# Kernel tuning notes

Hardware: AMD Instinct MI355X
Metric: run time of the kernel (lower is better)

## Reference

```python
import jax, jax.numpy as jnp
import numpy as np

EPS = 1e-5

def layernorm(x, g, b):
    mu = jnp.mean(x, axis=-1, keepdims=True)
    var = jnp.mean(jnp.square(x - mu), axis=-1, keepdims=True)
    return (x - mu) * jax.lax.rsqrt(var + EPS) * g + b

def setup_inputs() -> dict:
    key = jax.random.key(0)
    ks = jax.random.split(key, 12)
    B, T, C, H = 4, 2048, 1024, 8
    Dh = C // H          # 128
    Dff = 4 * C          # 4096
    s = 0.02
    return {
        "x":     jax.random.normal(ks[0], (B, T, C), jnp.float32),
        "wq":    jax.random.normal(ks[1], (H, C, Dh), jnp.float32) * s,
        "wk":    jax.random.normal(ks[2], (H, C, Dh), jnp.float32) * s,
        "wv":    jax.random.normal(ks[3], (H, C, Dh), jnp.float32) * s,
        "w1":    jax.random.normal(ks[4], (C, Dff), jnp.float32) * s,
        "b1":    jnp.zeros((Dff,), jnp.float32),
        "w2":    jax.random.normal(ks[5], (Dff, C), jnp.float32) * s,
        "b2":    jnp.zeros((C,), jnp.float32),
        "ln1_g": jnp.ones((C,), jnp.float32),
        "ln1_b": jnp.zeros((C,), jnp.float32),
        "ln2_g": jnp.ones((C,), jnp.float32),
        "ln2_b": jnp.zeros((C,), jnp.float32),
    }

def reference(x, wq, wk, wv, w1, b1, w2, b2, ln1_g, ln1_b, ln2_g, ln2_b):
    B, T, C = x.shape
    H, _, Dh = wq.shape
    # --- multi-head self-attention (pre-LN) ---
    h = layernorm(x, ln1_g, ln1_b)
    q = jnp.einsum("btc,hcd->bhtd", h, wq)
    k = jnp.einsum("btc,hcd->bhtd", h, wk)
    v = jnp.einsum("btc,hcd->bhtd", h, wv)
    # NOTE: original multiplies by sqrt(head_size) (not divide) -- kept faithful
    scores = jnp.einsum("bhtd,bhsd->bhts", q, k) * (Dh ** 0.5)
    attn = jax.nn.softmax(scores, axis=-1)
    # dropout(p=0.2) treated as identity (eval mode)
    o = jnp.einsum("bhts,bhsd->bhtd", attn, v)
    # concat heads along last dim: head h fills contiguous slice
    o = o.transpose(0, 2, 1, 3).reshape(B, T, H * Dh)
    x = x + o  # no output projection in original module
    # --- feed-forward (pre-LN) ---
    h2 = layernorm(x, ln2_g, ln2_b)
    ff = jax.nn.relu(h2 @ w1 + b1) @ w2 + b2
    return x + ff
```

## Files before the change

kernel.cpp:

```cpp
#include <hip/hip_runtime.h>
#include <hip/hip_bf16.h>
#include <math.h>

#define B_   4
#define T_   2048
#define C_   1024
#define H_   8
#define DH   128
#define DFF  4096
#define M_   (B_*T_)

typedef __attribute__((ext_vector_type(8))) short bf16x8;
typedef __attribute__((ext_vector_type(4))) float f32x4;
typedef __attribute__((ext_vector_type(2))) unsigned int u32x2;

#define SC2 16.32223094f

__device__ __forceinline__ unsigned short f2bf(float x) {
  union { float f; unsigned u; } v; v.f = x;
  return (unsigned short)((v.u + 0x7fffu + ((v.u >> 16) & 1u)) >> 16);
}
__device__ __forceinline__ float bf2f(unsigned short h) {
  union { unsigned u; float f; } v; v.u = ((unsigned)h) << 16; return v.f;
}

__device__ __forceinline__ f32x4 mfma_bf16(bf16x8 a, bf16x8 b, f32x4 c) {
  return __builtin_amdgcn_mfma_f32_16x16x32_bf16(a, b, c, 0, 0, 0);
}

__device__ __forceinline__ void gll16(const void* g, void* l) {
  __builtin_amdgcn_global_load_lds((const __attribute__((address_space(1))) void*)g,
                                   (__attribute__((address_space(3))) void*)l,
                                   16, 0, 0);
}

__global__ __launch_bounds__(256) void ln_kernel(const float* __restrict__ in,
                                                 const float* __restrict__ g,
                                                 const float* __restrict__ bb,
                                                 unsigned short* __restrict__ h_hi,
                                                 unsigned short* __restrict__ h_lo) {
  __shared__ float red[8];
  const int row = blockIdx.x;
  const int tid = threadIdx.x;
  const float* p = in + (size_t)row * C_;
  const float4 xv = *(const float4*)(p + (tid << 2));
  float s  = xv.x + xv.y + xv.z + xv.w;
  float sq = xv.x*xv.x + xv.y*xv.y + xv.z*xv.z + xv.w*xv.w;
  #pragma unroll
  for (int off = 32; off > 0; off >>= 1) {
    s  += __shfl_xor(s, off);
    sq += __shfl_xor(sq, off);
  }
  if ((tid & 63) == 0) { red[(tid >> 6) * 2] = s; red[(tid >> 6) * 2 + 1] = sq; }
  __syncthreads();
  s  = red[0] + red[2] + red[4] + red[6];
  sq = red[1] + red[3] + red[5] + red[7];
  const float mu  = s * (1.0f / C_);
  const float var = sq * (1.0f / C_) - mu * mu;
  const float rs  = rsqrtf(var + 1e-5f);
  const float4 gv = *(const float4*)(g  + (tid << 2));
  const float4 bv = *(const float4*)(bb + (tid << 2));
  float ov[4];
  ov[0] = (xv.x - mu) * rs * gv.x + bv.x;
  ov[1] = (xv.y - mu) * rs * gv.y + bv.y;
  ov[2] = (xv.z - mu) * rs * gv.z + bv.z;
  ov[3] = (xv.w - mu) * rs * gv.w + bv.w;
  ushort4 hv, lv;
  unsigned short* hp = (unsigned short*)&hv;
  unsigned short* lp = (unsigned short*)&lv;
  #pragma unroll
  for (int j = 0; j < 4; ++j) {
    hp[j] = f2bf(ov[j]);
    lp[j] = f2bf(ov[j] - bf2f(hp[j]));
  }
  *(ushort4*)(h_hi + (size_t)row * C_ + (tid << 2)) = hv;
  *(ushort4*)(h_lo + (size_t)row * C_ + (tid << 2)) = lv;
}

__global__ __launch_bounds__(256) void cvt_t_kernel(const float* __restrict__ in,
                                                    unsigned short* __restrict__ out,
                                                    int R, int CC) {
  __shared__ float tile[32][33];
  const int r0 = blockIdx.y << 5, c0 = blockIdx.x << 5;
  const int tr = threadIdx.x >> 3, tc4 = (threadIdx.x & 7) << 2;
  const float4 vv = *(const float4*)(in + (size_t)(r0 + tr) * CC + c0 + tc4);
  tile[tr][tc4+0] = vv.x; tile[tr][tc4+1] = vv.y;
  tile[tr][tc4+2] = vv.z; tile[tr][tc4+3] = vv.w;
  __syncthreads();
  ushort4 o;
  o.x = f2bf(tile[tc4+0][tr]); o.y = f2bf(tile[tc4+1][tr]);
  o.z = f2bf(tile[tc4+2][tr]); o.w = f2bf(tile[tc4+3][tr]);
  *(ushort4*)(out + (size_t)(c0 + tr) * R + r0 + tc4) = o;
}

__global__ __launch_bounds__(256) void cvt_qkv_kernel(const float* __restrict__ wq,
                                                      const float* __restrict__ wk,
                                                      const float* __restrict__ wv,
                                                      unsigned short* __restrict__ wt_hi,
                                                      unsigned short* __restrict__ wt_lo) {
  const int z = blockIdx.z;
  const int which = z >> 3, head = z & 7;
  const float* in = (which == 0 ? wq : (which == 1 ? wk : wv)) + (size_t)head * C_ * DH;
  unsigned short* oh = wt_hi + (size_t)z * DH * C_;
  unsigned short* ol = wt_lo + (size_t)z * DH * C_;
  __shared__ float tile[32][33];
  const int r0 = blockIdx.y << 5, c0 = blockIdx.x << 5;
  const int tr = threadIdx.x >> 3, tc4 = (threadIdx.x & 7) << 2;
  const float4 vv = *(const float4*)(in + (size_t)(r0 + tr) * DH + c0 + tc4);
  tile[tr][tc4+0] = vv.x; tile[tr][tc4+1] = vv.y;
  tile[tr][tc4+2] = vv.z; tile[tr][tc4+3] = vv.w;
  __syncthreads();
  ushort4 hv, lv;
  unsigned short* hp = (unsigned short*)&hv;
  unsigned short* lp = (unsigned short*)&lv;
  #pragma unroll
  for (int j = 0; j < 4; ++j) {
    const float val = tile[tc4+j][tr];
    hp[j] = f2bf(val);
    lp[j] = f2bf(val - bf2f(hp[j]));
  }
  *(ushort4*)(oh + (size_t)(c0 + tr) * C_ + r0 + tc4) = hv;
  *(ushort4*)(ol + (size_t)(c0 + tr) * C_ + r0 + tc4) = lv;
}

template<int TERMS>
__device__ __forceinline__ void gemm128_mfma(
    const unsigned short* __restrict__ Ah, const unsigned short* __restrict__ Al,
    int lda,
    const unsigned short* __restrict__ Bh, const unsigned short* __restrict__ Bl,
    int ldb, int K, f32x4 (&acc)[4][4],
    unsigned short* AhS, unsigned short* AlS,
    unsigned short* BhS, unsigned short* BlS) {
  const int tid  = threadIdx.x;
  const int w    = tid >> 6;
  const int lane = tid & 63;
  const int l15  = lane & 15, quad = lane >> 4;
  const int srow = lane >> 2, skc = (lane & 3) << 3;
  const int wm = w & 1, wn = w >> 1;

  for (int k0 = 0; k0 < K; k0 += 32) {
    __syncthreads();
    #pragma unroll
    for (int i = 0; i < 2; ++i) {
      const int seg  = w * 2 + i;
      const int r    = seg * 16 + srow;
      const int lofs = seg * 512 + lane * 8;
      gll16(Ah + (size_t)r * lda + k0 + skc, AhS + lofs);
      gll16(Bh + (size_t)r * ldb + k0 + skc, BhS + lofs);
      if (TERMS == 3) {
        gll16(Al + (size_t)r * lda + k0 + skc, AlS + lofs);
        gll16(Bl + (size_t)r * ldb + k0 + skc, BlS + lofs);
      }
    }
    __syncthreads();
    bf16x8 aH[4], bH[4], aL[4], bL[4];
    #pragma unroll
    for (int t = 0; t < 4; ++t) {
      aH[t] = *(const bf16x8*)&AhS[(wm * 64 + t * 16 + l15) * 32 + quad * 8];
      bH[t] = *(const bf16x8*)&BhS[(wn * 64 + t * 16 + l15) * 32 + quad * 8];
      if (TERMS == 3) {
        aL[t] = *(const bf16x8*)&AlS[(wm * 64 + t * 16 + l15) * 32 + quad * 8];
        bL[t] = *(const bf16x8*)&BlS[(wn * 64 + t * 16 + l15) * 32 + quad * 8];
      }
    }
    #pragma unroll
    for (int rt = 0; rt < 4; ++rt)
      #pragma unroll
      for (int ct = 0; ct < 4; ++ct) {
        if (TERMS == 3) {
          acc[rt][ct] = mfma_bf16(aL[rt], bH[ct], acc[rt][ct]);
          acc[rt][ct] = mfma_bf16(aH[rt], bL[ct], acc[rt][ct]);
        }
        acc[rt][ct] = mfma_bf16(aH[rt], bH[ct], acc[rt][ct]);
      }
  }
}

__global__ __launch_bounds__(256) void qkm_kernel(const unsigned short* __restrict__ h_hi,
                                                  const unsigned short* __restrict__ h_lo,
                                                  const unsigned short* __restrict__ wt_hi,
                                                  const unsigned short* __restrict__ wt_lo,
                                                  unsigned short* __restrict__ q_hi,
                                                  unsigned short* __restrict__ q_lo,
                                                  unsigned short* __restrict__ k_hi,
                                                  unsigned short* __restrict__ k_lo) {
  __shared__ __align__(16) unsigned short AhS[4096], AlS[4096];
  __shared__ __align__(16) unsigned short BhS[4096], BlS[4096];
  const int m0 = blockIdx.x << 7;
  const int z  = blockIdx.y;
  const int which = z >> 3, head = z & 7;
  f32x4 acc[4][4];
  #pragma unroll
  for (int i = 0; i < 4; ++i)
    #pragma unroll
    for (int j = 0; j < 4; ++j)
      #pragma unroll
      for (int r = 0; r < 4; ++r) acc[i][j][r] = 0.f;
  gemm128_mfma<3>(h_hi + (size_t)m0 * C_, h_lo + (size_t)m0 * C_, C_,
                  wt_hi + (size_t)z * DH * C_, wt_lo + (size_t)z * DH * C_, C_,
                  C_, acc, AhS, AlS, BhS, BlS);
  const int lane = threadIdx.x & 63, w = threadIdx.x >> 6;
  const int l15 = lane & 15, quad = lane >> 4;
  const int wm = w & 1, wn = w >> 1;
  const int bh = (m0 >> 11) * H_ + head;
  const int tbase = (m0 & (T_ - 1)) + wm * 64 + quad * 4;
  if (which == 0) {
    #pragma unroll
    for (int rt = 0; rt < 4; ++rt)
      #pragma unroll
      for (int ct = 0; ct < 4; ++ct) {
        const int d = wn * 64 + ct * 16 + l15;
        #pragma unroll
        for (int r = 0; r < 4; ++r) {
          const int t = tbase + rt * 16 + r;
          const float val = acc[rt][ct][r] * SC2;
          const unsigned short hb = f2bf(val);
          const size_t idx = ((size_t)bh * T_ + t) * DH + d;
          q_hi[idx] = hb;
          q_lo[idx] = f2bf(val - bf2f(hb));
        }
      }
  } else {
    #pragma unroll
    for (int rt = 0; rt < 4; ++rt)
      #pragma unroll
      for (int ct = 0; ct < 4; ++ct) {
        const int d = wn * 64 + ct * 16 + l15;
        #pragma unroll
        for (int r = 0; r < 4; ++r) {
          const int t = tbase + rt * 16 + r;
          const float val = acc[rt][ct][r];
          const unsigned short hb = f2bf(val);
          const size_t idx = (((size_t)bh * 64 + (t >> 5)) * 4 + (d >> 5)) * 1024
                           + (size_t)(t & 31) * 32 + (d & 31);
          k_hi[idx] = hb;
          k_lo[idx] = f2bf(val - bf2f(hb));
        }
      }
  }
}

__global__ __launch_bounds__(256) void vm_kernel(const unsigned short* __restrict__ h_hi,
                                                 const unsigned short* __restrict__ wv_hi,
                                                 unsigned short* __restrict__ vimg) {
  __shared__ __align__(16) unsigned short AhS[4096], BhS[4096];
  const int m0 = blockIdx.x << 7;
  const int head = blockIdx.y;
  f32x4 acc[4][4];
  #pragma unroll
  for (int i = 0; i < 4; ++i)
    #pragma unroll
    for (int j = 0; j < 4; ++j)
      #pragma unroll
      for (int r = 0; r < 4; ++r) acc[i][j][r] = 0.f;
  gemm128_mfma<1>(h_hi + (size_t)m0 * C_, nullptr, C_,
                  wv_hi + (size_t)(16 + head) * DH * C_, nullptr, C_,
                  C_, acc, AhS, nullptr, BhS, nullptr);
  const int lane = threadIdx.x & 63, w = threadIdx.x >> 6;
  const int l15 = lane & 15, quad = lane >> 4;
  const int wm = w & 1, wn = w >> 1;
  const int bh = (m0 >> 11) * H_ + head;
  #pragma unroll
  for (int rt = 0; rt < 4; ++rt)
    #pragma unroll
    for (int ct = 0; ct < 4; ++ct) {
      const int d  = wn * 64 + ct * 16 + l15;
      const int t0 = (m0 & (T_ - 1)) + wm * 64 + rt * 16 + quad * 4;
      ushort4 pk;
      pk.x = f2bf(acc[rt][ct][0]); pk.y = f2bf(acc[rt][ct][1]);
      pk.z = f2bf(acc[rt][ct][2]); pk.w = f2bf(acc[rt][ct][3]);
      *(ushort4*)&vimg[(((size_t)bh * 64 + (t0 >> 5)) * 128 + d) * 32 + (t0 & 31)] = pk;
    }
}

__global__ __launch_bounds__(256) void ff1_kernel(const unsigned short* __restrict__ h2,
                                                  const unsigned short* __restrict__ w1t,
                                                  const float* __restrict__ b1,
                                                  unsigned short* __restrict__ ff1) {
  __shared__ __align__(16) unsigned short AhS[4096], BhS[4096];
  const int n0 = blockIdx.x << 7;
  const int m0 = blockIdx.y << 7;
  f32x4 acc[4][4];
  #pragma unroll
  for (int i = 0; i < 4; ++i)
    #pragma unroll
    for (int j = 0; j < 4; ++j)
      #pragma unroll
      for (int r = 0; r < 4; ++r) acc[i][j][r] = 0.f;
  gemm128_mfma<1>(h2 + (size_t)m0 * C_, nullptr, C_,
                  w1t + (size_t)n0 * C_, nullptr, C_,
                  C_, acc, AhS, nullptr, BhS, nullptr);
  const int lane = threadIdx.x & 63, w = threadIdx.x >> 6;
  const int l15 = lane & 15, quad = lane >> 4;
  const int wm = w & 1, wn = w >> 1;
  #pragma unroll
  for (int rt = 0; rt < 4; ++rt)
    #pragma unroll
    for (int ct = 0; ct < 4; ++ct) {
      const int n = n0 + wn * 64 + ct * 16 + l15;
      const float bias = b1[n];
      #pragma unroll
      for (int r = 0; r < 4; ++r) {
        const int m = m0 + wm * 64 + rt * 16 + quad * 4 + r;
        ff1[(size_t)m * DFF + n] = f2bf(fmaxf(acc[rt][ct][r] + bias, 0.f));
      }
    }
}

__global__ __launch_bounds__(256) void ff2_kernel(const unsigned short* __restrict__ ff1,
                                                  const unsigned short* __restrict__ w2t,
                                                  const float* __restrict__ b2,
                                                  const float* __restrict__ xo,
                                                  float* __restrict__ out) {
  __shared__ __align__(16) unsigned short AhS[4096], BhS[4096];
  const int n0 = blockIdx.x << 7;
  const int m0 = blockIdx.y << 7;
  f32x4 acc[4][4];
  #pragma unroll
  for (int i = 0; i < 4; ++i)
    #pragma unroll
    for (int j = 0; j < 4; ++j)
      #pragma unroll
      for (int r = 0; r < 4; ++r) acc[i][j][r] = 0.f;
  gemm128_mfma<1>(ff1 + (size_t)m0 * DFF, nullptr, DFF,
                  w2t + (size_t)n0 * DFF, nullptr, DFF,
                  DFF, acc, AhS, nullptr, BhS, nullptr);
  const int lane = threadIdx.x & 63, w = threadIdx.x >> 6;
  const int l15 = lane & 15, quad = lane >> 4;
  const int wm = w & 1, wn = w >> 1;
  #pragma unroll
  for (int rt = 0; rt < 4; ++rt)
    #pragma unroll
    for (int ct = 0; ct < 4; ++ct) {
      const int n = n0 + wn * 64 + ct * 16 + l15;
      const float bias = b2[n];
      #pragma unroll
      for (int r = 0; r < 4; ++r) {
        const int m = m0 + wm * 64 + rt * 16 + quad * 4 + r;
        out[(size_t)m * C_ + n] = acc[rt][ct][r] + bias + xo[(size_t)m * C_ + n];
      }
    }
}

#define BQ 128

__global__ __launch_bounds__(256, 2) void attn_kernel(
    const unsigned short* __restrict__ q_hi, const unsigned short* __restrict__ q_lo,
    const unsigned short* __restrict__ k_hi, const unsigned short* __restrict__ k_lo,
    const unsigned short* __restrict__ vimg,
    const float* __restrict__ x, float* __restrict__ xo) {
  __shared__ __align__(16) unsigned short KhS[8192];
  __shared__ __align__(16) unsigned short KlS[8192];
  __shared__ __align__(16) unsigned short VtS[8192];
  __shared__ __align__(16) unsigned short PS [8192];

  const int bh  = blockIdx.y;
  const int qt0 = blockIdx.x * BQ;
  const int tid  = threadIdx.x;
  const int w    = tid >> 6;
  const int lane = tid & 63;
  const int l15  = lane & 15;
  const int quad = lane >> 4;
  const int srcbase = quad * 20;

  bf16x8 Qh[2][4], Ql[2][4];
  #pragma unroll
  for (int rt = 0; rt < 2; ++rt) {
    const int row = qt0 + w * 32 + rt * 16 + l15;
    #pragma unroll
    for (int kc = 0; kc < 4; ++kc) {
      const size_t off = ((size_t)bh * T_ + row) * DH + kc * 32 + quad * 8;
      Qh[rt][kc] = *(const bf16x8*)(q_hi + off);
      Ql[rt][kc] = *(const bf16x8*)(q_lo + off);
    }
  }

  f32x4 O[2][8];
  #pragma unroll
  for (int rt = 0; rt < 2; ++rt)
    #pragma unroll
    for (int n = 0; n < 8; ++n)
      #pragma unroll
      for (int r = 0; r < 4; ++r) O[rt][n][r] = 0.f;
  float m_cur[2] = { -1e30f, -1e30f };
  float l_cur[2] = { 0.f, 0.f };

  for (int kt = 0; kt < T_ / 64; ++kt) {
    const size_t tb = ((size_t)bh * 64 + kt * 2) * 4096;
    __syncthreads();
    #pragma unroll
    for (int i = 0; i < 4; ++i) {
      const int ofs = (w * 4 + i) * 512 + lane * 8;
      gll16(k_hi + tb + ofs, KhS + ofs);
      gll16(k_lo + tb + ofs, KlS + ofs);
      gll16(vimg + tb + ofs, VtS + ofs);
    }
    __syncthreads();

    f32x4 S[4][2];
    #pragma unroll
    for (int ct = 0; ct < 4; ++ct)
      #pragma unroll
      for (int rt = 0; rt < 2; ++rt)
        #pragma unroll
        for (int r = 0; r < 4; ++r) S[ct][rt][r] = 0.f;
    __builtin_amdgcn_s_setprio(1);
    #pragma unroll
    for (int kc = 0; kc < 4; ++kc) {
      #pragma unroll
      for (int ct = 0; ct < 4; ++ct) {
        const int o = (ct >> 1) * 4096 + kc * 1024 + (((ct & 1) << 4) + l15) * 32 + quad * 8;
        const bf16x8 kh = *(const bf16x8*)&KhS[o];
        const bf16x8 kl = *(const bf16x8*)&KlS[o];
        #pragma unroll
        for (int rt = 0; rt < 2; ++rt) {
          S[ct][rt] = mfma_bf16(kl, Qh[rt][kc], S[ct][rt]);
          S[ct][rt] = mfma_bf16(kh, Ql[rt][kc], S[ct][rt]);
          S[ct][rt] = mfma_bf16(kh, Qh[rt][kc], S[ct][rt]);
        }
      }
    }
    __builtin_amdgcn_s_setprio(0);

    float mx[2];
    #pragma unroll
    for (int rt = 0; rt < 2; ++rt) {
      const float c0 = fmaxf(fmaxf(S[0][rt][0], S[0][rt][1]), fmaxf(S[0][rt][2], S[0][rt][3]));
      const float c1 = fmaxf(fmaxf(S[1][rt][0], S[1][rt][1]), fmaxf(S[1][rt][2], S[1][rt][3]));
      const float c2 = fmaxf(fmaxf(S[2][rt][0], S[2][rt][1]), fmaxf(S[2][rt][2], S[2][rt][3]));
      const float c3 = fmaxf(fmaxf(S[3][rt][0], S[3][rt][1]), fmaxf(S[3][rt][2], S[3][rt][3]));
      float m0 = fmaxf(fmaxf(c0, c1), fmaxf(c2, c3));
      m0 = fmaxf(m0, __shfl_xor(m0, 16));
      m0 = fmaxf(m0, __shfl_xor(m0, 32));
      mx[rt] = m0;
    }

    const int need = (mx[0] > m_cur[0] + 8.f) || (mx[1] > m_cur[1] + 8.f);
    if (__any(need)) {
      #pragma unroll
      for (int rt = 0; rt < 2; ++rt) {
        const float mn = fmaxf(m_cur[rt], mx[rt]);
        const float al = exp2f(m_cur[rt] - mn);
        m_cur[rt] = mn;
        l_cur[rt] *= al;
        #pragma unroll
        for (int r = 0; r < 4; ++r) {
          const float ar = __shfl(al, srcbase + r);
          #pragma unroll
          for (int n = 0; n < 8; ++n) O[rt][n][r] *= ar;
        }
      }
    }

    #pragma unroll
    for (int rt = 0; rt < 2; ++rt) {
      const int rowb = (w * 32 + rt * 16 + l15) * 128;
      float rs = 0.f;
      #pragma unroll
      for (int ct = 0; ct < 4; ++ct) {
        const float p0 = exp2f(S[ct][rt][0] - m_cur[rt]);
        const float p1 = exp2f(S[ct][rt][1] - m_cur[rt]);
        const float p2 = exp2f(S[ct][rt][2] - m_cur[rt]);
        const float p3 = exp2f(S[ct][rt][3] - m_cur[rt]);
        rs += (p0 + p1) + (p2 + p3);
        u32x2 uu;
        uu.x = (__float_as_uint(p1) & 0xffff0000u) | (__float_as_uint(p0) >> 16);
        uu.y = (__float_as_uint(p3) & 0xffff0000u) | (__float_as_uint(p2) >> 16);
        const int slot = (ct * 2 + (quad >> 1)) ^ (l15 & 7);
        *(u32x2*)((char*)PS + rowb + (slot << 4) + ((quad & 1) << 3)) = uu;
      }
      rs += __shfl_xor(rs, 16);
      rs += __shfl_xor(rs, 32);
      l_cur[rt] += rs;
    }

    __builtin_amdgcn_s_setprio(1);
    #pragma unroll
    for (int kc = 0; kc < 2; ++kc) {
      bf16x8 aP[2];
      #pragma unroll
      for (int rt = 0; rt < 2; ++rt) {
        const int rowb = (w * 32 + rt * 16 + l15) * 128;
        const int slot = (kc * 4 + quad) ^ (l15 & 7);
        aP[rt] = *(const bf16x8*)((const char*)PS + rowb + (slot << 4));
      }
      #pragma unroll
      for (int n = 0; n < 8; ++n) {
        const bf16x8 bv = *(const bf16x8*)&VtS[kc * 4096 + (n * 16 + l15) * 32 + quad * 8];
        O[0][n] = mfma_bf16(aP[0], bv, O[0][n]);
        O[1][n] = mfma_bf16(aP[1], bv, O[1][n]);
      }
    }
    __builtin_amdgcn_s_setprio(0);
  }

  const int b = bh >> 3, hh = bh & 7;
  #pragma unroll
  for (int rt = 0; rt < 2; ++rt) {
    #pragma unroll
    for (int r = 0; r < 4; ++r) {
      const float lr = __shfl(l_cur[rt], srcbase + r);
      const float inv_l = 1.0f / lr;
      const int t = qt0 + w * 32 + rt * 16 + quad * 4 + r;
      const size_t xrow = ((size_t)(b * T_ + t)) * C_ + (size_t)hh * DH;
      #pragma unroll
      for (int n = 0; n < 8; ++n) {
        const int d = n * 16 + l15;
        xo[xrow + d] = x[xrow + d] + O[rt][n][r] * inv_l;
      }
    }
  }
}

extern "C" void kernel_launch(void* const* d_in, const int* in_sizes, int n_in,
                              void* d_out, int out_size, void* d_ws, size_t ws_size,
                              hipStream_t stream) {
  (void)in_sizes; (void)n_in; (void)out_size; (void)ws_size;
  const float* x     = (const float*)d_in[0];
  const float* wq    = (const float*)d_in[1];
  const float* wk    = (const float*)d_in[2];
  const float* wv    = (const float*)d_in[3];
  const float* w1    = (const float*)d_in[4];
  const float* b1    = (const float*)d_in[5];
  const float* w2    = (const float*)d_in[6];
  const float* b2    = (const float*)d_in[7];
  const float* ln1_g = (const float*)d_in[8];
  const float* ln1_b = (const float*)d_in[9];
  const float* ln2_g = (const float*)d_in[10];
  const float* ln2_b = (const float*)d_in[11];
  float* out = (float*)d_out;

  char* W = (char*)d_ws;
  float* xo = (float*)(W);
  unsigned short* q_hi  = (unsigned short*)(W + (32u  << 20));
  unsigned short* q_lo  = (unsigned short*)(W + (48u  << 20));
  unsigned short* k_hi  = (unsigned short*)(W + (64u  << 20));
  unsigned short* k_lo  = (unsigned short*)(W + (80u  << 20));
  unsigned short* vimg  = (unsigned short*)(W + (96u  << 20));
  unsigned short* ff1   = (unsigned short*)(W + (32u  << 20));
  unsigned short* h_hi  = (unsigned short*)(W + (112u << 20));
  unsigned short* h_lo  = (unsigned short*)(W + (128u << 20));
  unsigned short* w1t   = (unsigned short*)(W + (144u << 20));
  unsigned short* w2t   = (unsigned short*)(W + (152u << 20));
  unsigned short* wt_hi = (unsigned short*)(W + (160u << 20));
  unsigned short* wt_lo = (unsigned short*)(W + (166u << 20));

  cvt_t_kernel<<<dim3(DFF / 32, C_ / 32), 256, 0, stream>>>(w1, w1t, C_, DFF);
  cvt_t_kernel<<<dim3(C_ / 32, DFF / 32), 256, 0, stream>>>(w2, w2t, DFF, C_);
  cvt_qkv_kernel<<<dim3(DH / 32, C_ / 32, 24), 256, 0, stream>>>(wq, wk, wv, wt_hi, wt_lo);
  ln_kernel<<<M_, 256, 0, stream>>>(x, ln1_g, ln1_b, h_hi, h_lo);
  qkm_kernel<<<dim3(M_ / 128, 16), 256, 0, stream>>>(h_hi, h_lo, wt_hi, wt_lo,
                                                     q_hi, q_lo, k_hi, k_lo);
  vm_kernel<<<dim3(M_ / 128, H_), 256, 0, stream>>>(h_hi, wt_hi, vimg);
  attn_kernel<<<dim3(T_ / BQ, B_ * H_), 256, 0, stream>>>(q_hi, q_lo, k_hi, k_lo,
                                                          vimg, x, xo);
  ln_kernel<<<M_, 256, 0, stream>>>(xo, ln2_g, ln2_b, h_hi, h_lo);
  ff1_kernel<<<dim3(DFF / 128, M_ / 128), 256, 0, stream>>>(h_hi, w1t, b1, ff1);
  ff2_kernel<<<dim3(C_ / 128, M_ / 128), 256, 0, stream>>>(ff1, w2t, b2, xo, out);
}
```

Baseline: 616.5 us.

## Double-buffer GEMM and attention LDS tiles with XOR swizzle and block remap

Adds a double-buffered bf16 GEMM path (used for the V projection and both FFN GEMMs) that prefetches the next K-slice into a second LDS buffer while computing the current one. The flash-attention loop is reworked the same way, with 32-key tiles ping-ponged across two buffers. XOR swizzles are applied to LDS layouts and to the K/V global images to reduce bank conflicts, and attention blocks are remapped so consecutive blocks spread across heads. The extra LDS per block may lower occupancy, and the wrap-around prefetch on the last iteration loads data that is never used.

```diff
diff --git a/kernel.cpp b/kernel.cpp
--- a/kernel.cpp
+++ b/kernel.cpp
@@ -123,8 +123,8 @@
   *(ushort4*)(ol + (size_t)(c0 + tr) * C_ + r0 + tc4) = lv;
 }
 
-template<int TERMS>
-__device__ __forceinline__ void gemm128_mfma(
+
+__device__ __forceinline__ void gemm128_split3(
     const unsigned short* __restrict__ Ah, const unsigned short* __restrict__ Al,
     int lda,
     const unsigned short* __restrict__ Bh, const unsigned short* __restrict__ Bl,
@@ -135,8 +135,10 @@
   const int w    = tid >> 6;
   const int lane = tid & 63;
   const int l15  = lane & 15, quad = lane >> 4;
-  const int srow = lane >> 2, skc = (lane & 3) << 3;
+  const int srow = lane >> 2;
+  const int skc  = ((lane & 3) << 3) ^ (((srow >> 1) & 3) << 3);
   const int wm = w & 1, wn = w >> 1;
+  const int ro = ((quad ^ ((l15 >> 1) & 3)) << 3);
 
   for (int k0 = 0; k0 < K; k0 += 32) {
     __syncthreads();
@@ -147,32 +149,76 @@
       const int lofs = seg * 512 + lane * 8;
       gll16(Ah + (size_t)r * lda + k0 + skc, AhS + lofs);
       gll16(Bh + (size_t)r * ldb + k0 + skc, BhS + lofs);
-      if (TERMS == 3) {
-        gll16(Al + (size_t)r * lda + k0 + skc, AlS + lofs);
-        gll16(Bl + (size_t)r * ldb + k0 + skc, BlS + lofs);
-      }
+      gll16(Al + (size_t)r * lda + k0 + skc, AlS + lofs);
+      gll16(Bl + (size_t)r * ldb + k0 + skc, BlS + lofs);
     }
     __syncthreads();
     bf16x8 aH[4], bH[4], aL[4], bL[4];
     #pragma unroll
     for (int t = 0; t < 4; ++t) {
-      aH[t] = *(const bf16x8*)&AhS[(wm * 64 + t * 16 + l15) * 32 + quad * 8];
-      bH[t] = *(const bf16x8*)&BhS[(wn * 64 + t * 16 + l15) * 32 + quad * 8];
-      if (TERMS == 3) {
-        aL[t] = *(const bf16x8*)&AlS[(wm * 64 + t * 16 + l15) * 32 + quad * 8];
-        bL[t] = *(const bf16x8*)&BlS[(wn * 64 + t * 16 + l15) * 32 + quad * 8];
-      }
+      aH[t] = *(const bf16x8*)&AhS[(wm * 64 + t * 16 + l15) * 32 + ro];
+      bH[t] = *(const bf16x8*)&BhS[(wn * 64 + t * 16 + l15) * 32 + ro];
+      aL[t] = *(const bf16x8*)&AlS[(wm * 64 + t * 16 + l15) * 32 + ro];
+      bL[t] = *(const bf16x8*)&BlS[(wn * 64 + t * 16 + l15) * 32 + ro];
     }
     #pragma unroll
     for (int rt = 0; rt < 4; ++rt)
       #pragma unroll
       for (int ct = 0; ct < 4; ++ct) {
-        if (TERMS == 3) {
-          acc[rt][ct] = mfma_bf16(aL[rt], bH[ct], acc[rt][ct]);
-          acc[rt][ct] = mfma_bf16(aH[rt], bL[ct], acc[rt][ct]);
-        }
+        acc[rt][ct] = mfma_bf16(aL[rt], bH[ct], acc[rt][ct]);
+        acc[rt][ct] = mfma_bf16(aH[rt], bL[ct], acc[rt][ct]);
         acc[rt][ct] = mfma_bf16(aH[rt], bH[ct], acc[rt][ct]);
       }
+  }
+}
+
+__device__ __forceinline__ void gemm128_db(
+    const unsigned short* __restrict__ Ah, int lda,
+    const unsigned short* __restrict__ Bh, int ldb, int K, f32x4 (&acc)[4][4],
+    unsigned short (&AS0)[4096], unsigned short (&AS1)[4096],
+    unsigned short (&BS0)[4096], unsigned short (&BS1)[4096]) {
+  const int tid  = threadIdx.x;
+  const int w    = tid >> 6;
+  const int lane = tid & 63;
+  const int l15  = lane & 15, quad = lane >> 4;
+  const int srow = lane >> 2;
+  const int skc  = ((lane & 3) << 3) ^ (((srow >> 1) & 3) << 3);
+  const int wm = w & 1, wn = w >> 1;
+  const int ro = ((quad ^ ((l15 >> 1) & 3)) << 3);
+  const int Km = K - 1;
+
+  auto STG = [&](int k0, unsigned short* A, unsigned short* B) {
+    #pragma unroll
+    for (int i = 0; i < 2; ++i) {
+      const int seg  = w * 2 + i;
+      const int r    = seg * 16 + srow;
+      const int lofs = seg * 512 + lane * 8;
+      gll16(Ah + (size_t)r * lda + k0 + skc, A + lofs);
+      gll16(Bh + (size_t)r * ldb + k0 + skc, B + lofs);
+    }
+  };
+  auto CMP = [&](const unsigned short* A, const unsigned short* B) {
+    bf16x8 aH[4], bH[4];
+    #pragma unroll
+    for (int t = 0; t < 4; ++t) {
+      aH[t] = *(const bf16x8*)&A[(wm * 64 + t * 16 + l15) * 32 + ro];
+      bH[t] = *(const bf16x8*)&B[(wn * 64 + t * 16 + l15) * 32 + ro];
+    }
+    #pragma unroll
+    for (int rt = 0; rt < 4; ++rt)
+      #pragma unroll
+      for (int ct = 0; ct < 4; ++ct)
+        acc[rt][ct] = mfma_bf16(aH[rt], bH[ct], acc[rt][ct]);
+  };
+
+  STG(0, AS0, BS0);
+  for (int k0 = 0; k0 < K; k0 += 64) {
+    __syncthreads();
+    STG((k0 + 32) & Km, AS1, BS1);
+    CMP(AS0, BS0);
+    __syncthreads();
+    STG((k0 + 64) & Km, AS0, BS0);
+    CMP(AS1, BS1);
   }
 }
 
@@ -196,9 +242,9 @@
     for (int j = 0; j < 4; ++j)
       #pragma unroll
       for (int r = 0; r < 4; ++r) acc[i][j][r] = 0.f;
-  gemm128_mfma<3>(h_hi + (size_t)m0 * C_, h_lo + (size_t)m0 * C_, C_,
-                  wt_hi + (size_t)z * DH * C_, wt_lo + (size_t)z * DH * C_, C_,
-                  C_, acc, AhS, AlS, BhS, BlS);
+  gemm128_split3(h_hi + (size_t)m0 * C_, h_lo + (size_t)m0 * C_, C_,
+                 wt_hi + (size_t)z * DH * C_, wt_lo + (size_t)z * DH * C_, C_,
+                 C_, acc, AhS, AlS, BhS, BlS);
   const int lane = threadIdx.x & 63, w = threadIdx.x >> 6;
   const int l15 = lane & 15, quad = lane >> 4;
   const int wm = w & 1, wn = w >> 1;
@@ -229,10 +275,11 @@
         #pragma unroll
         for (int r = 0; r < 4; ++r) {
           const int t = tbase + rt * 16 + r;
+          const int tt = t & 31;
           const float val = acc[rt][ct][r];
           const unsigned short hb = f2bf(val);
           const size_t idx = (((size_t)bh * 64 + (t >> 5)) * 4 + (d >> 5)) * 1024
-                           + (size_t)(t & 31) * 32 + (d & 31);
+                           + (size_t)tt * 32 + ((d & 31) ^ (((tt >> 1) & 3) << 3));
           k_hi[idx] = hb;
           k_lo[idx] = f2bf(val - bf2f(hb));
         }
@@ -243,7 +290,8 @@
 __global__ __launch_bounds__(256) void vm_kernel(const unsigned short* __restrict__ h_hi,
                                                  const unsigned short* __restrict__ wv_hi,
                                                  unsigned short* __restrict__ vimg) {
-  __shared__ __align__(16) unsigned short AhS[4096], BhS[4096];
+  __shared__ __align__(16) unsigned short AS0[4096], AS1[4096];
+  __shared__ __align__(16) unsigned short BS0[4096], BS1[4096];
   const int m0 = blockIdx.x << 7;
   const int head = blockIdx.y;
   f32x4 acc[4][4];
@@ -253,9 +301,9 @@
     for (int j = 0; j < 4; ++j)
       #pragma unroll
       for (int r = 0; r < 4; ++r) acc[i][j][r] = 0.f;
-  gemm128_mfma<1>(h_hi + (size_t)m0 * C_, nullptr, C_,
-                  wv_hi + (size_t)(16 + head) * DH * C_, nullptr, C_,
-                  C_, acc, AhS, nullptr, BhS, nullptr);
+  gemm128_db(h_hi + (size_t)m0 * C_, C_,
+             wv_hi + (size_t)(16 + head) * DH * C_, C_,
+             C_, acc, AS0, AS1, BS0, BS1);
   const int lane = threadIdx.x & 63, w = threadIdx.x >> 6;
   const int l15 = lane & 15, quad = lane >> 4;
   const int wm = w & 1, wn = w >> 1;
@@ -266,10 +314,11 @@
     for (int ct = 0; ct < 4; ++ct) {
       const int d  = wn * 64 + ct * 16 + l15;
       const int t0 = (m0 & (T_ - 1)) + wm * 64 + rt * 16 + quad * 4;
+      const int key = (t0 & 31) ^ (((d >> 1) & 3) << 3);
       ushort4 pk;
       pk.x = f2bf(acc[rt][ct][0]); pk.y = f2bf(acc[rt][ct][1]);
       pk.z = f2bf(acc[rt][ct][2]); pk.w = f2bf(acc[rt][ct][3]);
-      *(ushort4*)&vimg[(((size_t)bh * 64 + (t0 >> 5)) * 128 + d) * 32 + (t0 & 31)] = pk;
+      *(ushort4*)&vimg[(((size_t)bh * 64 + (t0 >> 5)) * 128 + d) * 32 + key] = pk;
     }
 }
 
@@ -277,7 +326,8 @@
                                                   const unsigned short* __restrict__ w1t,
                                                   const float* __restrict__ b1,
                                                   unsigned short* __restrict__ ff1) {
-  __shared__ __align__(16) unsigned short AhS[4096], BhS[4096];
+  __shared__ __align__(16) unsigned short AS0[4096], AS1[4096];
+  __shared__ __align__(16) unsigned short BS0[4096], BS1[4096];
   const int n0 = blockIdx.x << 7;
   const int m0 = blockIdx.y << 7;
   f32x4 acc[4][4];
@@ -287,9 +337,9 @@
     for (int j = 0; j < 4; ++j)
       #pragma unroll
       for (int r = 0; r < 4; ++r) acc[i][j][r] = 0.f;
-  gemm128_mfma<1>(h2 + (size_t)m0 * C_, nullptr, C_,
-                  w1t + (size_t)n0 * C_, nullptr, C_,
-                  C_, acc, AhS, nullptr, BhS, nullptr);
+  gemm128_db(h2 + (size_t)m0 * C_, C_,
+             w1t + (size_t)n0 * C_, C_,
+             C_, acc, AS0, AS1, BS0, BS1);
   const int lane = threadIdx.x & 63, w = threadIdx.x >> 6;
   const int l15 = lane & 15, quad = lane >> 4;
   const int wm = w & 1, wn = w >> 1;
@@ -312,7 +362,8 @@
                                                   const float* __restrict__ b2,
                                                   const float* __restrict__ xo,
                                                   float* __restrict__ out) {
-  __shared__ __align__(16) unsigned short AhS[4096], BhS[4096];
+  __shared__ __align__(16) unsigned short AS0[4096], AS1[4096];
+  __shared__ __align__(16) unsigned short BS0[4096], BS1[4096];
   const int n0 = blockIdx.x << 7;
   const int m0 = blockIdx.y << 7;
   f32x4 acc[4][4];
@@ -322,9 +373,9 @@
     for (int j = 0; j < 4; ++j)
       #pragma unroll
       for (int r = 0; r < 4; ++r) acc[i][j][r] = 0.f;
-  gemm128_mfma<1>(ff1 + (size_t)m0 * DFF, nullptr, DFF,
-                  w2t + (size_t)n0 * DFF, nullptr, DFF,
-                  DFF, acc, AhS, nullptr, BhS, nullptr);
+  gemm128_db(ff1 + (size_t)m0 * DFF, DFF,
+             w2t + (size_t)n0 * DFF, DFF,
+             DFF, acc, AS0, AS1, BS0, BS1);
   const int lane = threadIdx.x & 63, w = threadIdx.x >> 6;
   const int l15 = lane & 15, quad = lane >> 4;
   const int wm = w & 1, wn = w >> 1;
@@ -349,18 +400,22 @@
     const unsigned short* __restrict__ k_hi, const unsigned short* __restrict__ k_lo,
     const unsigned short* __restrict__ vimg,
     const float* __restrict__ x, float* __restrict__ xo) {
-  __shared__ __align__(16) unsigned short KhS[8192];
-  __shared__ __align__(16) unsigned short KlS[8192];
-  __shared__ __align__(16) unsigned short VtS[8192];
-  __shared__ __align__(16) unsigned short PS [8192];
-
-  const int bh  = blockIdx.y;
-  const int qt0 = blockIdx.x * BQ;
+  __shared__ __align__(16) unsigned short Kh0[4096], Kh1[4096];
+  __shared__ __align__(16) unsigned short Kl0[4096], Kl1[4096];
+  __shared__ __align__(16) unsigned short Vt0[4096], Vt1[4096];
+  __shared__ __align__(16) unsigned short PS [4096];
+
+  const int bid   = blockIdx.x + (T_ / BQ) * blockIdx.y;
+  const int chunk = bid >> 3;
+  const int bh    = (bid & 7) * 4 + (chunk >> 4);
+  const int qt0   = (chunk & 15) * BQ;
+
   const int tid  = threadIdx.x;
   const int w    = tid >> 6;
   const int lane = tid & 63;
   const int l15  = lane & 15;
   const int quad = lane >> 4;
+  const int swz  = (l15 >> 1) & 3;
   const int srcbase = quad * 20;
 
   bf16x8 Qh[2][4], Ql[2][4];
@@ -385,21 +440,23 @@
   float m_cur[2] = { -1e30f, -1e30f };
   float l_cur[2] = { 0.f, 0.f };
 
-  for (int kt = 0; kt < T_ / 64; ++kt) {
-    const size_t tb = ((size_t)bh * 64 + kt * 2) * 4096;
-    __syncthreads();
-    #pragma unroll
-    for (int i = 0; i < 4; ++i) {
-      const int ofs = (w * 4 + i) * 512 + lane * 8;
-      gll16(k_hi + tb + ofs, KhS + ofs);
-      gll16(k_lo + tb + ofs, KlS + ofs);
-      gll16(vimg + tb + ofs, VtS + ofs);
-    }
-    __syncthreads();
-
-    f32x4 S[4][2];
-    #pragma unroll
-    for (int ct = 0; ct < 4; ++ct)
+  auto STAGE = [&](int kt, unsigned short* KH, unsigned short* KL,
+                   unsigned short* VT) {
+    const size_t tb = ((size_t)bh * 64 + kt) * 4096;
+    #pragma unroll
+    for (int i = 0; i < 2; ++i) {
+      const int ofs = (w * 2 + i) * 512 + lane * 8;
+      gll16(k_hi + tb + ofs, KH + ofs);
+      gll16(k_lo + tb + ofs, KL + ofs);
+      gll16(vimg + tb + ofs, VT + ofs);
+    }
+  };
+
+  auto TILE = [&](const unsigned short* KH, const unsigned short* KL,
+                  const unsigned short* VT) {
+    f32x4 S[2][2];
+    #pragma unroll
+    for (int ct = 0; ct < 2; ++ct)
       #pragma unroll
       for (int rt = 0; rt < 2; ++rt)
         #pragma unroll
@@ -408,10 +465,10 @@
     #pragma unroll
     for (int kc = 0; kc < 4; ++kc) {
       #pragma unroll
-      for (int ct = 0; ct < 4; ++ct) {
-        const int o = (ct >> 1) * 4096 + kc * 1024 + (((ct & 1) << 4) + l15) * 32 + quad * 8;
-        const bf16x8 kh = *(const bf16x8*)&KhS[o];
-        const bf16x8 kl = *(const bf16x8*)&KlS[o];
+      for (int ct = 0; ct < 2; ++ct) {
+        const int o = kc * 1024 + (ct * 16 + l15) * 32 + ((quad ^ swz) << 3);
+        const bf16x8 kh = *(const bf16x8*)&KH[o];
+        const bf16x8 kl = *(const bf16x8*)&KL[o];
         #pragma unroll
         for (int rt = 0; rt < 2; ++rt) {
           S[ct][rt] = mfma_bf16(kl, Qh[rt][kc], S[ct][rt]);
@@ -425,11 +482,11 @@
     float mx[2];
     #pragma unroll
     for (int rt = 0; rt < 2; ++rt) {
-      const float c0 = fmaxf(fmaxf(S[0][rt][0], S[0][rt][1]), fmaxf(S[0][rt][2], S[0][rt][3]));
-      const float c1 = fmaxf(fmaxf(S[1][rt][0], S[1][rt][1]), fmaxf(S[1][rt][2], S[1][rt][3]));
-      const float c2 = fmaxf(fmaxf(S[2][rt][0], S[2][rt][1]), fmaxf(S[2][rt][2], S[2][rt][3]));
-      const float c3 = fmaxf(fmaxf(S[3][rt][0], S[3][rt][1]), fmaxf(S[3][rt][2], S[3][rt][3]));
-      float m0 = fmaxf(fmaxf(c0, c1), fmaxf(c2, c3));
+      const float a = fmaxf(fmaxf(S[0][rt][0], S[0][rt][1]),
+                            fmaxf(S[0][rt][2], S[0][rt][3]));
+      const float b = fmaxf(fmaxf(S[1][rt][0], S[1][rt][1]),
+                            fmaxf(S[1][rt][2], S[1][rt][3]));
+      float m0 = fmaxf(a, b);
       m0 = fmaxf(m0, __shfl_xor(m0, 16));
       m0 = fmaxf(m0, __shfl_xor(m0, 32));
       mx[rt] = m0;
@@ -454,10 +511,10 @@
 
     #pragma unroll
     for (int rt = 0; rt < 2; ++rt) {
-      const int rowb = (w * 32 + rt * 16 + l15) * 128;
+      const int rowb = (w * 32 + rt * 16 + l15) * 64;
       float rs = 0.f;
       #pragma unroll
-      for (int ct = 0; ct < 4; ++ct) {
+      for (int ct = 0; ct < 2; ++ct) {
         const float p0 = exp2f(S[ct][rt][0] - m_cur[rt]);
         const float p1 = exp2f(S[ct][rt][1] - m_cur[rt]);
         const float p2 = exp2f(S[ct][rt][2] - m_cur[rt]);
@@ -466,7 +523,7 @@
         u32x2 uu;
         uu.x = (__float_as_uint(p1) & 0xffff0000u) | (__float_as_uint(p0) >> 16);
         uu.y = (__float_as_uint(p3) & 0xffff0000u) | (__float_as_uint(p2) >> 16);
-        const int slot = (ct * 2 + (quad >> 1)) ^ (l15 & 7);
+        const int slot = (ct * 2 + (quad >> 1)) ^ swz;
         *(u32x2*)((char*)PS + rowb + (slot << 4) + ((quad & 1) << 3)) = uu;
       }
       rs += __shfl_xor(rs, 16);
@@ -474,24 +531,32 @@
       l_cur[rt] += rs;
     }
 
+    bf16x8 aP[2];
+    #pragma unroll
+    for (int rt = 0; rt < 2; ++rt) {
+      const int rowb = (w * 32 + rt * 16 + l15) * 64;
+      aP[rt] = *(const bf16x8*)((const char*)PS + rowb + ((quad ^ swz) << 4));
+    }
     __builtin_amdgcn_s_setprio(1);
     #pragma unroll
-    for (int kc = 0; kc < 2; ++kc) {
-      bf16x8 aP[2];
-      #pragma unroll
-      for (int rt = 0; rt < 2; ++rt) {
-        const int rowb = (w * 32 + rt * 16 + l15) * 128;
-        const int slot = (kc * 4 + quad) ^ (l15 & 7);
-        aP[rt] = *(const bf16x8*)((const char*)PS + rowb + (slot << 4));
-      }
-      #pragma unroll
-      for (int n = 0; n < 8; ++n) {
-        const bf16x8 bv = *(const bf16x8*)&VtS[kc * 4096 + (n * 16 + l15) * 32 + quad * 8];
-        O[0][n] = mfma_bf16(aP[0], bv, O[0][n]);
-        O[1][n] = mfma_bf16(aP[1], bv, O[1][n]);
-      }
+    for (int n = 0; n < 8; ++n) {
+      const int o = (n * 16 + l15) * 32 + ((quad ^ swz) << 3);
+      const bf16x8 bv = *(const bf16x8*)&VT[o];
+      O[0][n] = mfma_bf16(aP[0], bv, O[0][n]);
+      O[1][n] = mfma_bf16(aP[1], bv, O[1][n]);
     }
     __builtin_amdgcn_s_setprio(0);
+  };
+
+  STAGE(0, Kh0, Kl0, Vt0);
+  for (int j = 0; j < T_ / 64; ++j) {
+    const int kt = j * 2;
+    __syncthreads();
+    STAGE(kt + 1, Kh1, Kl1, Vt1);
+    TILE(Kh0, Kl0, Vt0);
+    __syncthreads();
+    STAGE((kt + 2) & 63, Kh0, Kl0, Vt0);
+    TILE(Kh1, Kl1, Vt1);
   }
 
   const int b = bh >> 3, hh = bh & 7;
```

After: 632.1 us. 1.03x slower.
